# Kernel optimization log

Hardware: AMD Instinct MI355X
Metric: run time of the kernel (lower is better)

The kernel has to match this reference:

```python
import jax, jax.numpy as jnp
import numpy as np

HIDDEN = 2048
NUM_HEADS = 16
HEAD_DIM = 128
WINDOW = 256
BATCH = 2
SEQ = 2048
ROPE_BASE = 10000.0


def apply_rope(t):
    # t: [b, h, s, d]; half-split (rotate-half) rotary embedding
    d = t.shape[-1]
    s = t.shape[-2]
    inv_freq = 1.0 / (ROPE_BASE ** (jnp.arange(0, d, 2, dtype=jnp.float32) / d))  # [d/2]
    freqs = jnp.arange(s, dtype=jnp.float32)[:, None] * inv_freq[None, :]          # [s, d/2]
    cos, sin = jnp.cos(freqs), jnp.sin(freqs)
    t1, t2 = t[..., : d // 2], t[..., d // 2 :]
    return jnp.concatenate([t1 * cos - t2 * sin, t1 * sin + t2 * cos], axis=-1)


def setup_inputs() -> dict:
    key = jax.random.key(0)
    ks = jax.random.split(key, 10)
    dm = HEAD_DIM * NUM_HEADS
    lin_std = 1.0 / np.sqrt(HIDDEN)
    out_std = 1.0 / np.sqrt(dm)
    return {
        "x": jax.random.normal(ks[0], (BATCH, SEQ, HIDDEN), dtype=jnp.float32),
        "W_Q": jax.random.uniform(ks[1], (HIDDEN, dm), jnp.float32, -lin_std, lin_std),
        "b_Q": jax.random.uniform(ks[2], (dm,), jnp.float32, -lin_std, lin_std),
        "W_K": jax.random.uniform(ks[3], (HIDDEN, dm), jnp.float32, -lin_std, lin_std),
        "b_K": jax.random.uniform(ks[4], (dm,), jnp.float32, -lin_std, lin_std),
        "W_V": jax.random.uniform(ks[5], (HIDDEN, dm), jnp.float32, -lin_std, lin_std),
        "b_V": jax.random.uniform(ks[6], (dm,), jnp.float32, -lin_std, lin_std),
        "W_O": jax.random.uniform(ks[7], (dm, HIDDEN), jnp.float32, -out_std, out_std),
        "b_O": jax.random.uniform(ks[8], (HIDDEN,), jnp.float32, -out_std, out_std),
        "key_weights": jax.random.normal(ks[9], (NUM_HEADS,), dtype=jnp.float32),
    }


def reference(x, W_Q, b_Q, W_K, b_K, W_V, b_V, W_O, b_O, key_weights):
    b, s, _ = x.shape
    scale = HEAD_DIM ** -0.5

    def split_heads(t):  # [b, s, h*d] -> [b, h, s, d]
        return t.reshape(b, s, NUM_HEADS, HEAD_DIM).transpose(0, 2, 1, 3)

    q = split_heads(x @ W_Q + b_Q)
    k = split_heads(x @ W_K + b_K)
    v = split_heads(x @ W_V + b_V)

    q = apply_rope(q)
    k = apply_rope(k)

    # num_kv_heads == num_heads here, so group_size == 1: plain per-head attention
    scores = jnp.einsum("bhqd,bhkd->bhqk", q, k) * scale
    scores = scores * key_weights[None, :, None, None]

    # sliding-window causal mask: allow 0 <= i - j <= WINDOW
    i = jnp.arange(s)[:, None]
    j = jnp.arange(s)[None, :]
    allowed = (j <= i) & (j >= i - WINDOW)
    scores = jnp.where(allowed[None, None], scores, -jnp.inf)

    attn = jax.nn.softmax(scores, axis=-1)
    out = jnp.einsum("bhqk,bhkd->bhqd", attn, v)  # [b, h, s, d]
    out = out.transpose(0, 2, 1, 3).reshape(b, s, NUM_HEADS * HEAD_DIM)
    return out @ W_O + b_O
```

## Files before the change

### kernel.cpp

```cpp
#include <hip/hip_runtime.h>
#include <cstdint>

#define SEQn   2048
#define NHn    16
#define HDn    128
#define DMn    2048
#define HIDn   2048
#define BATCHn 2
#define WINn   256
#define MROWS  (BATCHn*SEQn)
#define WELEMS ((size_t)HIDn * DMn)

typedef short s16x8 __attribute__((ext_vector_type(8)));
typedef float f32x4 __attribute__((ext_vector_type(4)));

__device__ __forceinline__ float bf2f(ushort x) {
    union { uint u; float f; } v; v.u = ((uint)x) << 16; return v.f;
}
__device__ __forceinline__ ushort f2bf(float f) {
    union { float f; uint u; } v; v.f = f;
    uint u = v.u;
    return (ushort)((u + 0x7FFFu + ((u >> 16) & 1u)) >> 16);
}

#define GLOAD_LDS16(g, l) __builtin_amdgcn_global_load_lds(                   \
    (const __attribute__((address_space(1))) unsigned int*)(g),               \
    (__attribute__((address_space(3))) unsigned int*)(l), 16, 0, 0)

#define FENCE() do { asm volatile("" ::: "memory");                           \
                     __builtin_amdgcn_sched_barrier(0); } while (0)

__global__ __launch_bounds__(256)
void transpose_all_kernel(const float* __restrict__ WQ, const float* __restrict__ WK,
                          const float* __restrict__ WV, const float* __restrict__ WO,
                          ushort* __restrict__ WT,
                          const float* __restrict__ x, ushort* __restrict__ xb)
{
    const int tid = threadIdx.y * 32 + threadIdx.x;
    if (blockIdx.z == 4) {
        const int bid = blockIdx.y * 32 + blockIdx.x;
        const size_t b0 = (size_t)bid * 8192;
        #pragma unroll
        for (int i = 0; i < 4; ++i) {
            const size_t base = b0 + i * 2048 + tid * 8;
            const float4 a0 = *reinterpret_cast<const float4*>(x + base);
            const float4 a1 = *reinterpret_cast<const float4*>(x + base + 4);
            ushort4 o0, o1;
            o0.x = f2bf(a0.x); o0.y = f2bf(a0.y); o0.z = f2bf(a0.z); o0.w = f2bf(a0.w);
            o1.x = f2bf(a1.x); o1.y = f2bf(a1.y); o1.z = f2bf(a1.z); o1.w = f2bf(a1.w);
            *reinterpret_cast<ushort4*>(xb + base)     = o0;
            *reinterpret_cast<ushort4*>(xb + base + 4) = o1;
        }
        return;
    }
    __shared__ ushort t[64][76];
    const float* src = (blockIdx.z == 0) ? WQ : (blockIdx.z == 1) ? WK
                     : (blockIdx.z == 2) ? WV : WO;
    ushort* dst = WT + (size_t)blockIdx.z * WELEMS;
    const int n0 = blockIdx.x * 64;
    const int k0 = blockIdx.y * 64;
    const int c4 = (tid & 15) * 4;
    const int r0 = tid >> 4;
    #pragma unroll
    for (int i = 0; i < 4; ++i) {
        const int r = r0 + i * 16;
        const float4 a = *reinterpret_cast<const float4*>(
            src + (size_t)(k0 + r) * 2048 + n0 + c4);
        t[c4 + 0][r] = f2bf(a.x);
        t[c4 + 1][r] = f2bf(a.y);
        t[c4 + 2][r] = f2bf(a.z);
        t[c4 + 3][r] = f2bf(a.w);
    }
    __syncthreads();
    const int rowg = tid >> 4;
    const int kc   = (tid & 15) * 4;
    #pragma unroll
    for (int rr2 = 0; rr2 < 4; ++rr2) {
        const int arow = rowg + rr2 * 16;
        const ushort4 v = *reinterpret_cast<const ushort4*>(&t[arow][kc]);
        *reinterpret_cast<ushort4*>(dst + (size_t)(n0 + arow) * 2048 + k0 + kc) = v;
    }
}

__global__ __launch_bounds__(256)
void transpose_cvt_kernel(const float* __restrict__ src, ushort* __restrict__ dst)
{
    __shared__ ushort t[32][33];
    const int tx = threadIdx.x, ty = threadIdx.y;
    const int n  = blockIdx.x * 32 + tx;
    const int k0 = blockIdx.y * 32;
    #pragma unroll
    for (int r = ty; r < 32; r += 8)
        t[r][tx] = f2bf(src[(size_t)(k0 + r) * 2048 + n]);
    __syncthreads();
    const int k  = k0 + tx;
    const int nb = blockIdx.x * 32;
    #pragma unroll
    for (int r = ty; r < 32; r += 8)
        dst[(size_t)(nb + r) * 2048 + k] = t[tx][r];
}

template<int ABF16>
__global__ __launch_bounds__(256)
void gemm_qkv_kernel(const void* __restrict__ Araw, const ushort* __restrict__ WT,
                     const float* __restrict__ bQ, const float* __restrict__ bK,
                     const float* __restrict__ bV,
                     ushort* __restrict__ Qb, ushort* __restrict__ Kb,
                     ushort* __restrict__ Vt)
{
    __shared__ __align__(16) ushort smem[32768];
    const int tid = threadIdx.x;
    const int m0  = blockIdx.y * 128;
    const int n0g = blockIdx.x * 128;
    const int sel = n0g >> 11;
    const int n0  = n0g & 2047;
    const ushort* BT  = WT + (size_t)sel * WELEMS;
    const float* bias = (sel == 0) ? bQ : (sel == 1) ? bK : bV;
    const int w  = tid >> 6;
    const int l  = tid & 63;
    const int wy = w >> 1, wx = w & 1;
    const int q  = l >> 4, lm = l & 15;
    const int sw = lm & 7;

    f32x4 acc[4][4];
    #pragma unroll
    for (int i = 0; i < 4; ++i)
        #pragma unroll
        for (int j = 0; j < 4; ++j) acc[i][j] = (f32x4)0.0f;

    auto stage = [&](int slot, int kt) {
        ushort* AsS = smem + slot * 16384;
        ushort* BsS = AsS + 8192;
        if (ABF16) {
            #pragma unroll
            for (int it = 0; it < 4; ++it) {
                const int v = it * 256 + tid;
                const int r = v >> 3;
                const int cs = ((v & 7) ^ (r & 7)) << 3;
                const ushort* gA = (const ushort*)Araw + (size_t)(m0 + r) * HIDn + kt + cs;
                const ushort* gB = BT + (size_t)(n0 + r) * HIDn + kt + cs;
                GLOAD_LDS16(gA, AsS + (it * 256 + w * 64) * 8);
                GLOAD_LDS16(gB, BsS + (it * 256 + w * 64) * 8);
            }
        } else {
            #pragma unroll
            for (int it = 0; it < 4; ++it) {
                const int v = it * 256 + tid;
                const int r = v >> 3;
                const int c = (v & 7) << 3;
                const float* Af = (const float*)Araw + (size_t)(m0 + r) * HIDn + kt + c;
                const float4 a0 = *reinterpret_cast<const float4*>(Af);
                const float4 a1 = *reinterpret_cast<const float4*>(Af + 4);
                ushort* d = &AsS[(size_t)(v ^ (r & 7)) * 8];
                d[0] = f2bf(a0.x); d[1] = f2bf(a0.y); d[2] = f2bf(a0.z); d[3] = f2bf(a0.w);
                d[4] = f2bf(a1.x); d[5] = f2bf(a1.y); d[6] = f2bf(a1.z); d[7] = f2bf(a1.w);
                const int cs = ((v & 7) ^ (r & 7)) << 3;
                const ushort* gB = BT + (size_t)(n0 + r) * HIDn + kt + cs;
                GLOAD_LDS16(gB, BsS + (it * 256 + w * 64) * 8);
            }
        }
    };

    auto compute = [&](int slot) {
        const ushort* AsS = smem + slot * 16384;
        const ushort* BsS = AsS + 8192;
        #pragma unroll
        for (int ks = 0; ks < 2; ++ks) {
            s16x8 af[4], bfv[4];
            #pragma unroll
            for (int im = 0; im < 4; ++im) {
                const int arow = wy * 64 + im * 16 + lm;
                af[im] = *reinterpret_cast<const s16x8*>(
                    &AsS[arow * 64 + (((ks * 4 + q) ^ sw) << 3)]);
            }
            #pragma unroll
            for (int in = 0; in < 4; ++in) {
                const int brow = wx * 64 + in * 16 + lm;
                bfv[in] = *reinterpret_cast<const s16x8*>(
                    &BsS[brow * 64 + (((ks * 4 + q) ^ sw) << 3)]);
            }
            __builtin_amdgcn_s_setprio(1);
            #pragma unroll
            for (int im = 0; im < 4; ++im)
                #pragma unroll
                for (int in = 0; in < 4; ++in)
                    acc[im][in] = __builtin_amdgcn_mfma_f32_16x16x32_bf16(af[im], bfv[in], acc[im][in], 0, 0, 0);
            __builtin_amdgcn_s_setprio(0);
        }
    };

    const int NT = HIDn / 64;
    stage(0, 0);
    int cur = 0;
    for (int t = 0; t < NT - 1; ++t) {
        stage(cur ^ 1, (t + 1) * 64);
        if (ABF16) asm volatile("s_waitcnt vmcnt(8)" ::: "memory");
        else       asm volatile("s_waitcnt vmcnt(4)" ::: "memory");
        __builtin_amdgcn_s_barrier();
        FENCE();
        compute(cur);
        FENCE();
        if (!ABF16) asm volatile("s_waitcnt lgkmcnt(0)" ::: "memory");
        __builtin_amdgcn_s_barrier();
        FENCE();
        cur ^= 1;
    }
    asm volatile("s_waitcnt vmcnt(0)" ::: "memory");
    __builtin_amdgcn_s_barrier();
    FENCE();
    compute(cur);
    __syncthreads();

    if (sel == 2) {
        ushort* ctile = smem;
        #pragma unroll
        for (int in = 0; in < 4; ++in) {
            const int col = wx * 64 + in * 16 + lm;
            const float bv = bias[n0 + col];
            #pragma unroll
            for (int im = 0; im < 4; ++im) {
                const int row0 = wy * 64 + im * 16 + q * 4;
                #pragma unroll
                for (int r = 0; r < 4; ++r)
                    ctile[col * 136 + row0 + r] = f2bf(acc[im][in][r] + bv);
            }
        }
        __syncthreads();
        const int hh = n0 >> 7;
        const int bb = m0 >> 11;
        const int s0 = m0 & (SEQn - 1);
        const int st = (tid & 15) * 8;
        const int d0 = tid >> 4;
        #pragma unroll
        for (int db = 0; db < 8; ++db) {
            const int d = d0 + db * 16;
            const ushort4 v0 = *reinterpret_cast<const ushort4*>(&ctile[d * 136 + st]);
            const ushort4 v1 = *reinterpret_cast<const ushort4*>(&ctile[d * 136 + st + 4]);
            ushort* dstp = Vt + (((size_t)(bb * NHn + hh)) * HDn + d) * SEQn + s0 + st;
            *reinterpret_cast<ushort4*>(dstp)     = v0;
            *reinterpret_cast<ushort4*>(dstp + 4) = v1;
        }
    } else {
        ushort* ctile = smem;
        #pragma unroll
        for (int in = 0; in < 4; ++in) {
            const int col = wx * 64 + in * 16 + lm;
            const float bv = bias[n0 + col];
            #pragma unroll
            for (int im = 0; im < 4; ++im) {
                const int row0 = wy * 64 + im * 16 + q * 4;
                #pragma unroll
                for (int r = 0; r < 4; ++r)
                    ctile[(row0 + r) * 136 + col] = f2bf(acc[im][in][r] + bv);
            }
        }
        __syncthreads();
        ushort* dst = (sel == 0) ? Qb : Kb;
        const int d = tid & 63;
        const float invf = exp2f(-(float)d * 0.20762050593046f);
        for (int r = tid >> 6; r < 128; r += 4) {
            const int s = (m0 + r) & (SEQn - 1);
            const float ang = (float)s * invf;
            float sn, cs;
            __sincosf(ang, &sn, &cs);
            const float t1 = bf2f(ctile[r * 136 + d]);
            const float t2 = bf2f(ctile[r * 136 + 64 + d]);
            const size_t base = (size_t)(m0 + r) * DMn + n0 + d;
            dst[base]      = f2bf(t1 * cs - t2 * sn);
            dst[base + 64] = f2bf(t1 * sn + t2 * cs);
        }
    }
}

__global__ __launch_bounds__(256)
void gemm_out_kernel(const ushort* __restrict__ A, const ushort* __restrict__ BT,
                     const float* __restrict__ bias, float* __restrict__ C)
{
    __shared__ __align__(16) ushort smem[32768];
    const int tid = threadIdx.x;
    const int m0 = blockIdx.y * 128;
    const int n0 = blockIdx.x * 128;
    const int w  = tid >> 6;
    const int l  = tid & 63;
    const int wy = w >> 1, wx = w & 1;
    const int q  = l >> 4, lm = l & 15;
    const int sw = lm & 7;

    f32x4 acc[4][4];
    #pragma unroll
    for (int i = 0; i < 4; ++i)
        #pragma unroll
        for (int j = 0; j < 4; ++j) acc[i][j] = (f32x4)0.0f;

    auto stage = [&](int slot, int kt) {
        ushort* AsS = smem + slot * 16384;
        ushort* BsS = AsS + 8192;
        #pragma unroll
        for (int it = 0; it < 4; ++it) {
            const int v = it * 256 + tid;
            const int r = v >> 3;
            const int cs = ((v & 7) ^ (r & 7)) << 3;
            GLOAD_LDS16(A  + (size_t)(m0 + r) * DMn + kt + cs,
                        AsS + (it * 256 + w * 64) * 8);
            GLOAD_LDS16(BT + (size_t)(n0 + r) * DMn + kt + cs,
                        BsS + (it * 256 + w * 64) * 8);
        }
    };

    auto compute = [&](int slot) {
        const ushort* AsS = smem + slot * 16384;
        const ushort* BsS = AsS + 8192;
        #pragma unroll
        for (int ks = 0; ks < 2; ++ks) {
            s16x8 af[4], bfv[4];
            #pragma unroll
            for (int im = 0; im < 4; ++im) {
                const int arow = wy * 64 + im * 16 + lm;
                af[im] = *reinterpret_cast<const s16x8*>(
                    &AsS[arow * 64 + (((ks * 4 + q) ^ sw) << 3)]);
            }
            #pragma unroll
            for (int in = 0; in < 4; ++in) {
                const int brow = wx * 64 + in * 16 + lm;
                bfv[in] = *reinterpret_cast<const s16x8*>(
                    &BsS[brow * 64 + (((ks * 4 + q) ^ sw) << 3)]);
            }
            __builtin_amdgcn_s_setprio(1);
            #pragma unroll
            for (int im = 0; im < 4; ++im)
                #pragma unroll
                for (int in = 0; in < 4; ++in)
                    acc[im][in] = __builtin_amdgcn_mfma_f32_16x16x32_bf16(af[im], bfv[in], acc[im][in], 0, 0, 0);
            __builtin_amdgcn_s_setprio(0);
        }
    };

    const int NT = DMn / 64;
    stage(0, 0);
    int cur = 0;
    for (int t = 0; t < NT - 1; ++t) {
        stage(cur ^ 1, (t + 1) * 64);
        asm volatile("s_waitcnt vmcnt(8)" ::: "memory");
        __builtin_amdgcn_s_barrier();
        FENCE();
        compute(cur);
        FENCE();
        __builtin_amdgcn_s_barrier();
        FENCE();
        cur ^= 1;
    }
    asm volatile("s_waitcnt vmcnt(0)" ::: "memory");
    __builtin_amdgcn_s_barrier();
    FENCE();
    compute(cur);

    #pragma unroll
    for (int in = 0; in < 4; ++in) {
        const int gcol = n0 + wx * 64 + in * 16 + lm;
        const float bv = bias[gcol];
        #pragma unroll
        for (int im = 0; im < 4; ++im) {
            const int grow0 = m0 + wy * 64 + im * 16 + q * 4;
            #pragma unroll
            for (int r = 0; r < 4; ++r)
                C[(size_t)(grow0 + r) * HIDn + gcol] = acc[im][in][r] + bv;
        }
    }
}

__global__ __launch_bounds__(256)
void attn_mfma_kernel(const ushort* Q, const ushort* __restrict__ K,
                      const ushort* __restrict__ Vt, const float* __restrict__ kw,
                      ushort* AO)
{
    __shared__ ushort plds[4][2][16 * 40];
    const int w  = threadIdx.x >> 6;
    const int l  = threadIdx.x & 63;
    const int q  = l >> 4, lm = l & 15;
    const int bid = blockIdx.x;
    const int swzb = (bid & 7) * 64 + (bid >> 3);
    const int gw = swzb * 4 + w;
    const int qt2 = gw & 63;
    const int h  = (gw >> 6) & (NHn - 1);
    const int b  = gw >> 10;
    const int q0 = qt2 * 32;
    const float f = kw[h] * 0.08838834764831845f;

    s16x8 qfA[4], qfB[4];
    const size_t qbaseA = ((size_t)(b * SEQn + q0 + lm)) * DMn + h * HDn;
    const size_t qbaseB = qbaseA + (size_t)16 * DMn;
    #pragma unroll
    for (int ks = 0; ks < 4; ++ks) {
        qfA[ks] = *reinterpret_cast<const s16x8*>(Q + qbaseA + ks * 32 + q * 8);
        qfB[ks] = *reinterpret_cast<const s16x8*>(Q + qbaseB + ks * 32 + q * 8);
    }

    f32x4 OA[8], OB[8];
    #pragma unroll
    for (int nt = 0; nt < 8; ++nt) { OA[nt] = (f32x4)0.0f; OB[nt] = (f32x4)0.0f; }
    float mA[4], mB[4], lA[4], lB[4];
    #pragma unroll
    for (int r = 0; r < 4; ++r) { mA[r] = -1e30f; mB[r] = -1e30f; lA[r] = 0.f; lB[r] = 0.f; }

    const int lo = q0 - WINn;
    const int c0 = lo > 0 ? lo : 0;
    const int nch = (q0 + 32 - c0) >> 5;

    const size_t kbh = ((size_t)(b * SEQn)) * DMn + h * HDn;
    const size_t vbh = ((size_t)(b * NHn + h)) * HDn * SEQn;

    for (int c = 0; c < nch; ++c) {
        const int kc = c0 + c * 32;
        s16x8 vf[8], kf0[4], kf1[4];
        #pragma unroll
        for (int nt = 0; nt < 8; ++nt)
            vf[nt] = *reinterpret_cast<const s16x8*>(
                Vt + vbh + (size_t)(nt * 16 + lm) * SEQn + kc + q * 8);
        {
            const size_t krow0 = kbh + (size_t)(kc + lm) * DMn;
            const size_t krow1 = kbh + (size_t)(kc + 16 + lm) * DMn;
            #pragma unroll
            for (int ks = 0; ks < 4; ++ks) {
                kf0[ks] = *reinterpret_cast<const s16x8*>(K + krow0 + ks * 32 + q * 8);
                kf1[ks] = *reinterpret_cast<const s16x8*>(K + krow1 + ks * 32 + q * 8);
            }
        }
        f32x4 SA[2], SB[2];
        {
            f32x4 aA0 = (f32x4)0.0f, aB0 = (f32x4)0.0f;
            f32x4 aA1 = (f32x4)0.0f, aB1 = (f32x4)0.0f;
            __builtin_amdgcn_s_setprio(1);
            #pragma unroll
            for (int ks = 0; ks < 4; ++ks) {
                aA0 = __builtin_amdgcn_mfma_f32_16x16x32_bf16(qfA[ks], kf0[ks], aA0, 0, 0, 0);
                aB0 = __builtin_amdgcn_mfma_f32_16x16x32_bf16(qfB[ks], kf0[ks], aB0, 0, 0, 0);
                aA1 = __builtin_amdgcn_mfma_f32_16x16x32_bf16(qfA[ks], kf1[ks], aA1, 0, 0, 0);
                aB1 = __builtin_amdgcn_mfma_f32_16x16x32_bf16(qfB[ks], kf1[ks], aB1, 0, 0, 0);
            }
            __builtin_amdgcn_s_setprio(0);
            SA[0] = aA0; SA[1] = aA1; SB[0] = aB0; SB[1] = aB1;
        }
        const int j0 = kc + lm, j1 = kc + 16 + lm;
        #pragma unroll
        for (int r = 0; r < 4; ++r) {
            {
                const int i = q0 + q * 4 + r;
                float v0 = SA[0][r] * f;
                float v1 = SA[1][r] * f;
                if (j0 > i || j0 < i - WINn) v0 = -1e30f;
                if (j1 > i || j1 < i - WINn) v1 = -1e30f;
                float mx = fmaxf(v0, v1);
                #pragma unroll
                for (int off = 8; off > 0; off >>= 1)
                    mx = fmaxf(mx, __shfl_xor(mx, off));
                const float mn = fmaxf(mA[r], mx);
                const float alpha = __expf(mA[r] - mn);
                mA[r] = mn;
                const ushort h0 = f2bf(__expf(v0 - mn));
                const ushort h1 = f2bf(__expf(v1 - mn));
                plds[w][0][(q * 4 + r) * 40 + lm]      = h0;
                plds[w][0][(q * 4 + r) * 40 + 16 + lm] = h1;
                float ps = bf2f(h0) + bf2f(h1);
                #pragma unroll
                for (int off = 8; off > 0; off >>= 1)
                    ps += __shfl_xor(ps, off);
                lA[r] = lA[r] * alpha + ps;
                #pragma unroll
                for (int nt = 0; nt < 8; ++nt) OA[nt][r] *= alpha;
            }
            {
                const int i = q0 + 16 + q * 4 + r;
                float v0 = SB[0][r] * f;
                float v1 = SB[1][r] * f;
                if (j0 > i || j0 < i - WINn) v0 = -1e30f;
                if (j1 > i || j1 < i - WINn) v1 = -1e30f;
                float mx = fmaxf(v0, v1);
                #pragma unroll
                for (int off = 8; off > 0; off >>= 1)
                    mx = fmaxf(mx, __shfl_xor(mx, off));
                const float mn = fmaxf(mB[r], mx);
                const float alpha = __expf(mB[r] - mn);
                mB[r] = mn;
                const ushort h0 = f2bf(__expf(v0 - mn));
                const ushort h1 = f2bf(__expf(v1 - mn));
                plds[w][1][(q * 4 + r) * 40 + lm]      = h0;
                plds[w][1][(q * 4 + r) * 40 + 16 + lm] = h1;
                float ps = bf2f(h0) + bf2f(h1);
                #pragma unroll
                for (int off = 8; off > 0; off >>= 1)
                    ps += __shfl_xor(ps, off);
                lB[r] = lB[r] * alpha + ps;
                #pragma unroll
                for (int nt = 0; nt < 8; ++nt) OB[nt][r] *= alpha;
            }
        }
        const s16x8 pfA = *reinterpret_cast<const s16x8*>(&plds[w][0][lm * 40 + q * 8]);
        const s16x8 pfB = *reinterpret_cast<const s16x8*>(&plds[w][1][lm * 40 + q * 8]);
        __builtin_amdgcn_s_setprio(1);
        #pragma unroll
        for (int nt = 0; nt < 8; ++nt) {
            OA[nt] = __builtin_amdgcn_mfma_f32_16x16x32_bf16(pfA, vf[nt], OA[nt], 0, 0, 0);
            OB[nt] = __builtin_amdgcn_mfma_f32_16x16x32_bf16(pfB, vf[nt], OB[nt], 0, 0, 0);
        }
        __builtin_amdgcn_s_setprio(0);
    }
    #pragma unroll
    for (int r = 0; r < 4; ++r) {
        const float invA = 1.0f / lA[r];
        const float invB = 1.0f / lB[r];
        const size_t orowA = ((size_t)(b * SEQn + q0 + q * 4 + r)) * DMn + h * HDn;
        const size_t orowB = orowA + (size_t)16 * DMn;
        #pragma unroll
        for (int nt = 0; nt < 8; ++nt) {
            AO[orowA + nt * 16 + lm] = f2bf(OA[nt][r] * invA);
            AO[orowB + nt * 16 + lm] = f2bf(OB[nt][r] * invB);
        }
    }
}

extern "C" void kernel_launch(void* const* d_in, const int* in_sizes, int n_in,
                              void* d_out, int out_size, void* d_ws, size_t ws_size,
                              hipStream_t stream)
{
    (void)in_sizes; (void)n_in; (void)out_size;
    const float* x  = (const float*)d_in[0];
    const float* WQ = (const float*)d_in[1];
    const float* bQ = (const float*)d_in[2];
    const float* WK = (const float*)d_in[3];
    const float* bK = (const float*)d_in[4];
    const float* WV = (const float*)d_in[5];
    const float* bV = (const float*)d_in[6];
    const float* WO = (const float*)d_in[7];
    const float* bO = (const float*)d_in[8];
    const float* kw = (const float*)d_in[9];
    float* out = (float*)d_out;

    char* ws = (char*)d_ws;
    const size_t AELEMS = (size_t)MROWS * DMn;
    ushort* Qb = (ushort*)ws;
    ushort* Kb = (ushort*)(ws + AELEMS * 2);
    ushort* Vt = (ushort*)(ws + AELEMS * 4);
    ushort* WT = (ushort*)(ws + AELEMS * 6);
    const size_t FULL = AELEMS * 6 + WELEMS * 8 + AELEMS * 2;
    const bool have_full = ws_size >= FULL;
    ushort* xb = (ushort*)(ws + AELEMS * 6 + WELEMS * 8);

    const dim3 tblk(32, 8);
    const int attn_grid = BATCHn * NHn * (SEQn / 32) / 4;

    if (have_full) {
        transpose_all_kernel<<<dim3(32, 32, 5), tblk, 0, stream>>>(WQ, WK, WV, WO, WT, x, xb);
        gemm_qkv_kernel<1><<<dim3(3 * DMn / 128, MROWS / 128), 256, 0, stream>>>(
            xb, WT, bQ, bK, bV, Qb, Kb, Vt);
        attn_mfma_kernel<<<dim3(attn_grid), 256, 0, stream>>>(Qb, Kb, Vt, kw, Qb);
        gemm_out_kernel<<<dim3(HIDn / 128, MROWS / 128), 256, 0, stream>>>(
            Qb, WT + 3 * WELEMS, bO, out);
    } else {
        transpose_all_kernel<<<dim3(32, 32, 3), tblk, 0, stream>>>(WQ, WK, WV, WO, WT, x, xb);
        gemm_qkv_kernel<0><<<dim3(3 * DMn / 128, MROWS / 128), 256, 0, stream>>>(
            x, WT, bQ, bK, bV, Qb, Kb, Vt);
        attn_mfma_kernel<<<dim3(attn_grid), 256, 0, stream>>>(Qb, Kb, Vt, kw, Qb);
        transpose_cvt_kernel<<<dim3(64, 64), tblk, 0, stream>>>(WO, WT);
        gemm_out_kernel<<<dim3(HIDn / 128, MROWS / 128), 256, 0, stream>>>(Qb, WT, bO, out);
    }
}
```

Baseline: 344.0 us.

## Use 256x256-tile, 512-thread QKV GEMM with phased prefetch pipeline

Replaces the 128x128, 256-thread QKV projection GEMM with a 256x256 tile kernel on 8 waves. Each k-step is split into four phases that interleave global-to-LDS staging of the A and B halves with MFMA work. The larger tile halves global traffic per FLOP and improves operand reuse. In exchange it uses 128KB of LDS and more accumulator registers per thread, which limits occupancy, and it adds more barriers per k-step. The bf16-input path of the old templated kernel is removed because the new kernel now handles that case.

```diff
diff --git a/kernel.cpp b/kernel.cpp
--- a/kernel.cpp
+++ b/kernel.cpp
@@ -98,6 +98,194 @@
     #pragma unroll
     for (int r = ty; r < 32; r += 8)
         dst[(size_t)(nb + r) * 2048 + k] = t[tx][r];
+}
+
+__global__ __launch_bounds__(512, 2)
+void gemm_qkv_8ph(const ushort* __restrict__ A, const ushort* __restrict__ WT,
+                  const float* __restrict__ bQ, const float* __restrict__ bK,
+                  const float* __restrict__ bV,
+                  ushort* __restrict__ Qb, ushort* __restrict__ Kb,
+                  ushort* __restrict__ Vt)
+{
+    __shared__ __align__(16) ushort smem[65536];
+    const int tid = threadIdx.x;
+    const int m0  = blockIdx.y * 256;
+    const int n0g = blockIdx.x * 256;
+    const int sel = n0g >> 11;
+    const int n0  = n0g & 2047;
+    const ushort* BT  = WT + (size_t)sel * WELEMS;
+    const float* bias = (sel == 0) ? bQ : (sel == 1) ? bK : bV;
+    const int w  = tid >> 6;
+    const int l  = tid & 63;
+    const int wy = w >> 2;
+    const int wx = w & 3;
+    const int q  = l >> 4, lm = l & 15;
+    const int sw = lm & 7;
+
+    f32x4 acc[8][4];
+    #pragma unroll
+    for (int i = 0; i < 8; ++i)
+        #pragma unroll
+        for (int j = 0; j < 4; ++j) acc[i][j] = (f32x4)0.0f;
+
+    auto stageA = [&](int buf, int h, int kt) {
+        ushort* dst = smem + buf * 16384 + h * 8192;
+        #pragma unroll
+        for (int it = 0; it < 2; ++it) {
+            const int v = it * 512 + tid;
+            const int r = v >> 3;
+            const int cs = ((v & 7) ^ (r & 7)) << 3;
+            GLOAD_LDS16(A + (size_t)(m0 + h * 128 + r) * HIDn + kt + cs,
+                        dst + (it * 512 + w * 64) * 8);
+        }
+    };
+    auto stageB = [&](int buf, int h, int kt) {
+        ushort* dst = smem + 32768 + buf * 16384 + h * 8192;
+        #pragma unroll
+        for (int it = 0; it < 2; ++it) {
+            const int v = it * 512 + tid;
+            const int r = v >> 3;
+            const int cs = ((v & 7) ^ (r & 7)) << 3;
+            GLOAD_LDS16(BT + (size_t)(n0 + h * 128 + r) * HIDn + kt + cs,
+                        dst + (it * 512 + w * 64) * 8);
+        }
+    };
+
+    const int NT = HIDn / 64;
+    stageA(0, 0, 0);  stageA(0, 1, 0);  stageB(0, 0, 0);  stageB(0, 1, 0);
+    stageA(1, 0, 64); stageA(1, 1, 64); stageB(1, 0, 64); stageB(1, 1, 64);
+    asm volatile("s_waitcnt vmcnt(8)" ::: "memory");
+    __builtin_amdgcn_s_barrier();
+    FENCE();
+
+    for (int t = 0; t < NT; ++t) {
+        const int X = t & 1;
+        const ushort* Ah = smem + X * 16384 + wy * 8192;
+        const ushort* Bh = smem + 32768 + X * 16384 + (wx >> 1) * 8192;
+        const int brow0 = (wx & 1) * 64;
+        s16x8 bf[4][2];
+        #pragma unroll
+        for (int p = 0; p < 4; ++p) {
+            if (p == 0) {
+                #pragma unroll
+                for (int in = 0; in < 4; ++in)
+                    #pragma unroll
+                    for (int ks = 0; ks < 2; ++ks)
+                        bf[in][ks] = *reinterpret_cast<const s16x8*>(
+                            &Bh[(brow0 + in * 16 + lm) * 64 + (((ks * 4 + q) ^ sw) << 3)]);
+            }
+            s16x8 af[2][2];
+            #pragma unroll
+            for (int i2 = 0; i2 < 2; ++i2)
+                #pragma unroll
+                for (int ks = 0; ks < 2; ++ks)
+                    af[i2][ks] = *reinterpret_cast<const s16x8*>(
+                        &Ah[((p * 2 + i2) * 16 + lm) * 64 + (((ks * 4 + q) ^ sw) << 3)]);
+            if (p == 0)      { if (t >= 1 && t + 1 < NT) stageA(X ^ 1, 0, (t + 1) * 64); }
+            else if (p == 1) { if (t >= 1 && t + 1 < NT) stageA(X ^ 1, 1, (t + 1) * 64); }
+            else if (p == 2) { if (t + 2 < NT)           stageB(X, 0, (t + 2) * 64); }
+            else {
+                if (t + 2 < NT) stageB(X, 1, (t + 2) * 64);
+                if (t + 1 < NT) {
+                    if (t <= NT - 3) asm volatile("s_waitcnt vmcnt(4)" ::: "memory");
+                    else             asm volatile("s_waitcnt vmcnt(0)" ::: "memory");
+                }
+            }
+            FENCE();
+            __builtin_amdgcn_s_barrier();
+            asm volatile("s_waitcnt lgkmcnt(0)" ::: "memory");
+            FENCE();
+            __builtin_amdgcn_s_setprio(1);
+            #pragma unroll
+            for (int ks = 0; ks < 2; ++ks)
+                #pragma unroll
+                for (int i2 = 0; i2 < 2; ++i2)
+                    #pragma unroll
+                    for (int in = 0; in < 4; ++in)
+                        acc[p * 2 + i2][in] = __builtin_amdgcn_mfma_f32_16x16x32_bf16(
+                            af[i2][ks], bf[in][ks], acc[p * 2 + i2][in], 0, 0, 0);
+            __builtin_amdgcn_s_setprio(0);
+            FENCE();
+            __builtin_amdgcn_s_barrier();
+            FENCE();
+        }
+    }
+    __syncthreads();
+
+    if (sel == 2) {
+        #pragma unroll
+        for (int rr = 0; rr < 2; ++rr) {
+            if (wy == rr) {
+                #pragma unroll
+                for (int in = 0; in < 4; ++in) {
+                    const int col = wx * 64 + in * 16 + lm;
+                    const float bv = bias[n0 + col];
+                    #pragma unroll
+                    for (int im = 0; im < 8; ++im) {
+                        const int row0 = im * 16 + q * 4;
+                        #pragma unroll
+                        for (int r = 0; r < 4; ++r)
+                            smem[col * 136 + row0 + r] = f2bf(acc[im][in][r] + bv);
+                    }
+                }
+            }
+            __syncthreads();
+            const int bb = m0 >> 11;
+            const int sb = (m0 & (SEQn - 1)) + rr * 128;
+            const int st = (tid & 15) * 8;
+            const int c0i = tid >> 4;
+            #pragma unroll
+            for (int j = 0; j < 8; ++j) {
+                const int col = c0i + j * 32;
+                const int hh  = (n0 >> 7) + (col >> 7);
+                const int dd  = col & 127;
+                const ushort4 v0 = *reinterpret_cast<const ushort4*>(&smem[col * 136 + st]);
+                const ushort4 v1 = *reinterpret_cast<const ushort4*>(&smem[col * 136 + st + 4]);
+                ushort* dstp = Vt + (((size_t)(bb * NHn + hh)) * HDn + dd) * SEQn + sb + st;
+                *reinterpret_cast<ushort4*>(dstp)     = v0;
+                *reinterpret_cast<ushort4*>(dstp + 4) = v1;
+            }
+            __syncthreads();
+        }
+    } else {
+        ushort* dst = (sel == 0) ? Qb : Kb;
+        const int d = tid & 63;
+        const float invf = exp2f(-(float)d * 0.20762050593046f);
+        #pragma unroll
+        for (int rr = 0; rr < 2; ++rr) {
+            if (wy == rr) {
+                #pragma unroll
+                for (int in = 0; in < 4; ++in) {
+                    const int col = wx * 64 + in * 16 + lm;
+                    const float bv = bias[n0 + col];
+                    #pragma unroll
+                    for (int im = 0; im < 8; ++im) {
+                        const int row0 = im * 16 + q * 4;
+                        #pragma unroll
+                        for (int r = 0; r < 4; ++r)
+                            smem[(row0 + r) * 264 + col] = f2bf(acc[im][in][r] + bv);
+                    }
+                }
+            }
+            __syncthreads();
+            for (int lr = tid >> 6; lr < 128; lr += 8) {
+                const int grow = m0 + rr * 128 + lr;
+                const int s = grow & (SEQn - 1);
+                const float ang = (float)s * invf;
+                float sn, cs;
+                __sincosf(ang, &sn, &cs);
+                #pragma unroll
+                for (int hh2 = 0; hh2 < 2; ++hh2) {
+                    const float t1 = bf2f(smem[lr * 264 + hh2 * 128 + d]);
+                    const float t2 = bf2f(smem[lr * 264 + hh2 * 128 + 64 + d]);
+                    const size_t base = (size_t)grow * DMn + n0 + hh2 * 128 + d;
+                    dst[base]      = f2bf(t1 * cs - t2 * sn);
+                    dst[base + 64] = f2bf(t1 * sn + t2 * cs);
+                }
+            }
+            __syncthreads();
+        }
+    }
 }
 
 template<int ABF16>
@@ -131,33 +319,20 @@
     auto stage = [&](int slot, int kt) {
         ushort* AsS = smem + slot * 16384;
         ushort* BsS = AsS + 8192;
-        if (ABF16) {
-            #pragma unroll
-            for (int it = 0; it < 4; ++it) {
-                const int v = it * 256 + tid;
-                const int r = v >> 3;
-                const int cs = ((v & 7) ^ (r & 7)) << 3;
-                const ushort* gA = (const ushort*)Araw + (size_t)(m0 + r) * HIDn + kt + cs;
-                const ushort* gB = BT + (size_t)(n0 + r) * HIDn + kt + cs;
-                GLOAD_LDS16(gA, AsS + (it * 256 + w * 64) * 8);
-                GLOAD_LDS16(gB, BsS + (it * 256 + w * 64) * 8);
-            }
-        } else {
-            #pragma unroll
-            for (int it = 0; it < 4; ++it) {
-                const int v = it * 256 + tid;
-                const int r = v >> 3;
-                const int c = (v & 7) << 3;
-                const float* Af = (const float*)Araw + (size_t)(m0 + r) * HIDn + kt + c;
-                const float4 a0 = *reinterpret_cast<const float4*>(Af);
-                const float4 a1 = *reinterpret_cast<const float4*>(Af + 4);
-                ushort* d = &AsS[(size_t)(v ^ (r & 7)) * 8];
-                d[0] = f2bf(a0.x); d[1] = f2bf(a0.y); d[2] = f2bf(a0.z); d[3] = f2bf(a0.w);
-                d[4] = f2bf(a1.x); d[5] = f2bf(a1.y); d[6] = f2bf(a1.z); d[7] = f2bf(a1.w);
-                const int cs = ((v & 7) ^ (r & 7)) << 3;
-                const ushort* gB = BT + (size_t)(n0 + r) * HIDn + kt + cs;
-                GLOAD_LDS16(gB, BsS + (it * 256 + w * 64) * 8);
-            }
+        #pragma unroll
+        for (int it = 0; it < 4; ++it) {
+            const int v = it * 256 + tid;
+            const int r = v >> 3;
+            const int c = (v & 7) << 3;
+            const float* Af = (const float*)Araw + (size_t)(m0 + r) * HIDn + kt + c;
+            const float4 a0 = *reinterpret_cast<const float4*>(Af);
+            const float4 a1 = *reinterpret_cast<const float4*>(Af + 4);
+            ushort* d = &AsS[(size_t)(v ^ (r & 7)) * 8];
+            d[0] = f2bf(a0.x); d[1] = f2bf(a0.y); d[2] = f2bf(a0.z); d[3] = f2bf(a0.w);
+            d[4] = f2bf(a1.x); d[5] = f2bf(a1.y); d[6] = f2bf(a1.z); d[7] = f2bf(a1.w);
+            const int cs = ((v & 7) ^ (r & 7)) << 3;
+            const ushort* gB = BT + (size_t)(n0 + r) * HIDn + kt + cs;
+            GLOAD_LDS16(gB, BsS + (it * 256 + w * 64) * 8);
         }
     };
 
@@ -194,13 +369,12 @@
     int cur = 0;
     for (int t = 0; t < NT - 1; ++t) {
         stage(cur ^ 1, (t + 1) * 64);
-        if (ABF16) asm volatile("s_waitcnt vmcnt(8)" ::: "memory");
-        else       asm volatile("s_waitcnt vmcnt(4)" ::: "memory");
+        asm volatile("s_waitcnt vmcnt(4)" ::: "memory");
         __builtin_amdgcn_s_barrier();
         FENCE();
         compute(cur);
         FENCE();
-        if (!ABF16) asm volatile("s_waitcnt lgkmcnt(0)" ::: "memory");
+        asm volatile("s_waitcnt lgkmcnt(0)" ::: "memory");
         __builtin_amdgcn_s_barrier();
         FENCE();
         cur ^= 1;
@@ -550,7 +724,7 @@
 
     if (have_full) {
         transpose_all_kernel<<<dim3(32, 32, 5), tblk, 0, stream>>>(WQ, WK, WV, WO, WT, x, xb);
-        gemm_qkv_kernel<1><<<dim3(3 * DMn / 128, MROWS / 128), 256, 0, stream>>>(
+        gemm_qkv_8ph<<<dim3(3 * DMn / 256, MROWS / 256), 512, 0, stream>>>(
             xb, WT, bQ, bK, bV, Qb, Kb, Vt);
         attn_mfma_kernel<<<dim3(attn_grid), 256, 0, stream>>>(Qb, Kb, Vt, kw, Qb);
         gemm_out_kernel<<<dim3(HIDn / 128, MROWS / 128), 256, 0, stream>>>(
```

Result: slower. 359.5 us (+4.5%).
